# Performance work log

Measured on AMD Instinct MI355X. Metric: run time of the kernel, lower is better.

The kernel has to match this reference:

```python
import jax, jax.numpy as jnp
import numpy as np

B, T, D = 4, 2048, 512
H, DK = 4, 16
MU = 1.0


def _xavier(key, shape):
    lim = float(np.sqrt(6.0 / (shape[0] + shape[1])))
    return jax.random.uniform(key, shape, jnp.float32, -lim, lim)


def setup_inputs() -> dict:
    key = jax.random.key(0)
    ks = jax.random.split(key, 9)
    x = jax.random.normal(ks[0], (B, T, D), jnp.float32)
    Wq = _xavier(ks[1], (D, H * DK))
    Wk = _xavier(ks[2], (D, H * DK))
    Wv = _xavier(ks[3], (D, H * DK))
    # W_a is zero-initialized in the module; use small random values so the
    # decay path is exercised non-trivially.
    Wa = 0.02 * jax.random.normal(ks[4], (D, H), jnp.float32)
    ba = 0.02 * jax.random.normal(ks[5], (H,), jnp.float32)
    Wg = 0.02 * jax.random.normal(ks[6], (D, H * DK), jnp.float32)
    bg = jnp.zeros((H * DK,), jnp.float32)
    Wo = _xavier(ks[7], (H * DK, D))
    return {"x": x, "Wq": Wq, "Wk": Wk, "Wv": Wv, "Wa": Wa, "ba": ba,
            "Wg": Wg, "bg": bg, "Wo": Wo}


def reference(x, Wq, Wk, Wv, Wa, ba, Wg, bg, Wo):
    b_, t_, _ = x.shape
    q = (x @ Wq).reshape(b_, t_, H, DK)
    k = (x @ Wk).reshape(b_, t_, H, DK)
    v = (x @ Wv).reshape(b_, t_, H, DK)
    # bid b_s = <q_s, k_s>/sqrt(dk); decay a_s = -softplus(x W_a + c_a) <= 0
    bid = jnp.sum(q * k, axis=-1) / np.sqrt(DK)      # (B, T, H)
    a = -jax.nn.softplus(x @ Wa + ba)                # (B, T, H)
    # Closed form of the sequential scan:
    #   scores[t, s] = bid[s] + sum_{r=s+1..t} a[r] = (bid[s] - cumA[s]) + cumA[t]
    # Row-constant cumA[t] cancels in the softmax, so the attention weights are
    # a causal softmax over mu * (bid[s] - cumA[s]).
    cumA = jnp.cumsum(a, axis=1)                     # (B, T, H)
    lg = (bid - cumA).transpose(0, 2, 1)             # (B, H, S_keys)
    mask = jnp.tril(jnp.ones((t_, t_), bool))        # keys s <= query t
    scores = jnp.where(mask[None, None], MU * lg[:, :, None, :], -jnp.inf)
    w = jax.nn.softmax(scores, axis=-1)              # (B, H, T, S)
    y = jnp.einsum('bhts,bshd->bthd', w, v)          # (B, T, H, DK)
    gate = jax.nn.sigmoid(x @ Wg + bg).reshape(b_, t_, H, DK)
    y = (y * gate).reshape(b_, t_, H * DK)
    return y @ Wo
```

## Files before the change

kernel.cpp:

```cpp
#include <hip/hip_runtime.h>
#include <math.h>

#define B_    4
#define T_    2048
#define D_    512
#define H_    4
#define ROWS_ 8192
#define CHSZ_ 128
#define NCHK_ 16

typedef unsigned short ushort_t;
typedef unsigned int   uint_t;
typedef __attribute__((ext_vector_type(8))) __bf16         bfx8;
typedef __attribute__((ext_vector_type(8))) unsigned short u16x8;
typedef __attribute__((ext_vector_type(4))) float          fx4;

__device__ __forceinline__ ushort_t f2bf(float f) {
    union { float f; uint_t u; } v; v.f = f;
    return (ushort_t)((v.u + 0x7FFFu + ((v.u >> 16) & 1u)) >> 16);
}
__device__ __forceinline__ float bf2f(ushort_t u) {
    union { uint_t u; float f; } v; v.u = ((uint_t)u) << 16; return v.f;
}

__global__ __launch_bounds__(256) void prep_pack(const float* __restrict__ x,
                                                 const float* __restrict__ Wa,
                                                 const float* __restrict__ ba,
                                                 const float* __restrict__ Wq,
                                                 const float* __restrict__ Wk,
                                                 const float* __restrict__ Wv,
                                                 const float* __restrict__ Wg,
                                                 const float* __restrict__ Wo,
                                                 ushort_t* __restrict__ xbf,
                                                 float* __restrict__ Aarr,
                                                 ushort_t* __restrict__ WcatT2,
                                                 ushort_t* __restrict__ WoT) {
    const int blk = blockIdx.x;
    if (blk < 2048) {
        const int wave = threadIdx.x >> 6, lane = threadIdx.x & 63;
        const int row = blk * 4 + wave;
        const float* xp = x + (size_t)row * D_ + lane * 8;
        float4 f0 = *(const float4*)xp;
        float4 f1 = *(const float4*)(xp + 4);
        float xv[8] = {f0.x, f0.y, f0.z, f0.w, f1.x, f1.y, f1.z, f1.w};

        u16x8 u;
        #pragma unroll
        for (int j = 0; j < 8; j++) u[j] = f2bf(xv[j]);
        *(u16x8*)(xbf + (size_t)row * D_ + lane * 8) = u;

        float a0 = 0.f, a1 = 0.f, a2 = 0.f, a3 = 0.f;
        #pragma unroll
        for (int j = 0; j < 8; j++) {
            float4 w = *(const float4*)&Wa[(size_t)(lane * 8 + j) * 4];
            a0 = fmaf(xv[j], w.x, a0);
            a1 = fmaf(xv[j], w.y, a1);
            a2 = fmaf(xv[j], w.z, a2);
            a3 = fmaf(xv[j], w.w, a3);
        }
        #pragma unroll
        for (int off = 32; off; off >>= 1) {
            a0 += __shfl_xor(a0, off);
            a1 += __shfl_xor(a1, off);
            a2 += __shfl_xor(a2, off);
            a3 += __shfl_xor(a3, off);
        }
        if (lane == 0) {
            float z[4] = {a0 + ba[0], a1 + ba[1], a2 + ba[2], a3 + ba[3]};
            float r[4];
            #pragma unroll
            for (int h = 0; h < 4; h++)
                r[h] = -(fmaxf(z[h], 0.f) + log1pf(expf(-fabsf(z[h]))));
            *(float4*)&Aarr[(size_t)row * 4] = make_float4(r[0], r[1], r[2], r[3]);
        }
    } else {
        int idx = (blk - 2048) * 256 + threadIdx.x;
        if (idx < 256 * 512) {
            int n = idx >> 9, d = idx & 511;
            int h = n >> 6, r = n & 63, part = r >> 4, j = r & 15;
            int col = h * 16 + j;
            const float* W = (part == 0) ? Wq : (part == 1) ? Wk : (part == 2) ? Wv : Wg;
            WcatT2[idx] = f2bf(W[(size_t)d * 64 + col]);
        } else {
            int r = idx - 256 * 512;
            int n = r >> 6, k = r & 63;
            WoT[r] = f2bf(Wo[(size_t)k * 512 + n]);
        }
    }
}

__global__ __launch_bounds__(256) void gemm_scanA(const ushort_t* __restrict__ xbf,
                                                  const ushort_t* __restrict__ WcatT2,
                                                  const float* __restrict__ Aarr,
                                                  float* __restrict__ stateWS,
                                                  float* __restrict__ chunkSum,
                                                  ushort_t* __restrict__ gBuf) {
    __shared__ ushort_t As[128 * 72];
    __shared__ ushort_t Bs[64 * 72];
    __shared__ float s_a0;
    __shared__ float s_wmax[2];
    __shared__ float s_tot[17];

    const int rc = blockIdx.x & 63;
    const int h  = blockIdx.x >> 6;
    const int m0 = rc * 128;
    const int n0 = h * 64;
    const int b  = rc >> 4, chunk = rc & 15;
    const int bh = b * 4 + h;

    const int tid = threadIdx.x;
    const int wave = tid >> 6, lane = tid & 63;
    const int fr = lane & 15, quad = lane >> 4;
    const int sr = tid >> 3, sc = (tid & 7) * 8;

    fx4 acc[2][4];
    #pragma unroll
    for (int i = 0; i < 2; i++)
        #pragma unroll
        for (int j = 0; j < 4; j++) acc[i][j] = (fx4)0.f;

    u16x8 ra[4], rb[2];
    #pragma unroll
    for (int s = 0; s < 4; s++)
        ra[s] = *(const u16x8*)(xbf + (size_t)(m0 + s * 32 + sr) * D_ + sc);
    #pragma unroll
    for (int s = 0; s < 2; s++)
        rb[s] = *(const u16x8*)(WcatT2 + (size_t)(n0 + s * 32 + sr) * D_ + sc);

    for (int it = 0; it < 8; it++) {
        #pragma unroll
        for (int s = 0; s < 4; s++) *(u16x8*)&As[(s * 32 + sr) * 72 + sc] = ra[s];
        #pragma unroll
        for (int s = 0; s < 2; s++) *(u16x8*)&Bs[(s * 32 + sr) * 72 + sc] = rb[s];
        __syncthreads();
        if (it < 7) {
            const int k0 = (it + 1) * 64;
            #pragma unroll
            for (int s = 0; s < 4; s++)
                ra[s] = *(const u16x8*)(xbf + (size_t)(m0 + s * 32 + sr) * D_ + k0 + sc);
            #pragma unroll
            for (int s = 0; s < 2; s++)
                rb[s] = *(const u16x8*)(WcatT2 + (size_t)(n0 + s * 32 + sr) * D_ + k0 + sc);
        }
        #pragma unroll
        for (int ks = 0; ks < 64; ks += 32) {
            bfx8 af[2], bfr[4];
            #pragma unroll
            for (int mi = 0; mi < 2; mi++)
                af[mi] = *(const bfx8*)&As[(wave * 32 + mi * 16 + fr) * 72 + ks + quad * 8];
            #pragma unroll
            for (int ni = 0; ni < 4; ni++)
                bfr[ni] = *(const bfx8*)&Bs[(ni * 16 + fr) * 72 + ks + quad * 8];
            #pragma unroll
            for (int mi = 0; mi < 2; mi++)
                #pragma unroll
                for (int ni = 0; ni < 4; ni++)
                    acc[mi][ni] = __builtin_amdgcn_mfma_f32_16x16x32_bf16(af[mi], bfr[ni], acc[mi][ni], 0, 0, 0);
        }
        __syncthreads();
    }

    #pragma unroll
    for (int mi = 0; mi < 2; mi++)
        #pragma unroll
        for (int ni = 0; ni < 4; ni++)
            #pragma unroll
            for (int r = 0; r < 4; r++) {
                int rl = wave * 32 + mi * 16 + quad * 4 + r;
                int cl = ni * 16 + fr;
                As[rl * 72 + cl] = f2bf(acc[mi][ni][r]);
            }
    __syncthreads();

    const bool active = (tid < 128);
    float bid = 0.f, a = 0.f;
    float v[16];
    if (active) {
        const ushort_t* ct = &As[tid * 72];
        u16x8 q0 = *(const u16x8*)(ct +  0), q1 = *(const u16x8*)(ct +  8);
        u16x8 k0 = *(const u16x8*)(ct + 16), k1 = *(const u16x8*)(ct + 24);
        u16x8 v0 = *(const u16x8*)(ct + 32), v1 = *(const u16x8*)(ct + 40);
        #pragma unroll
        for (int j = 0; j < 8; j++) {
            bid = fmaf(bf2f(q0[j]), bf2f(k0[j]), bid);
            bid = fmaf(bf2f(q1[j]), bf2f(k1[j]), bid);
            v[j]     = bf2f(v0[j]);
            v[8 + j] = bf2f(v1[j]);
        }
        bid *= 0.25f;
        a = Aarr[(size_t)(m0 + tid) * 4 + h];
    }

    float ca = a;
    #pragma unroll
    for (int off = 1; off < 64; off <<= 1) {
        float up = __shfl_up(ca, off);
        if (lane >= off) ca += up;
    }
    if (tid == 63) s_a0 = ca;
    __syncthreads();
    if (active && wave == 1) ca += s_a0;

    float lg = bid - ca;

    float Mw = active ? lg : -1e30f;
    #pragma unroll
    for (int off = 32; off; off >>= 1) Mw = fmaxf(Mw, __shfl_xor(Mw, off));
    if (active && lane == 0) s_wmax[wave] = Mw;
    __syncthreads();
    const float M0 = s_wmax[0], M1 = s_wmax[1];
    const float Mc = fmaxf(M0, M1);

    float d = active ? __expf(lg - Mw) : 0.f;
    float n[16];
    #pragma unroll
    for (int j = 0; j < 16; j++) n[j] = d * v[j];
    #pragma unroll
    for (int off = 1; off < 64; off <<= 1) {
        float ud = __shfl_up(d, off);
        float un[16];
        #pragma unroll
        for (int j = 0; j < 16; j++) un[j] = __shfl_up(n[j], off);
        if (lane >= off) {
            d += ud;
            #pragma unroll
            for (int j = 0; j < 16; j++) n[j] += un[j];
        }
    }
    if (tid == 63) {
        s_tot[0] = d;
        #pragma unroll
        for (int j = 0; j < 16; j++) s_tot[1 + j] = n[j];
    }
    __syncthreads();
    if (active && wave == 1) {
        float al = __expf(M0 - Mc), be = __expf(M1 - Mc);
        d = s_tot[0] * al + d * be;
        #pragma unroll
        for (int j = 0; j < 16; j++) n[j] = s_tot[1 + j] * al + n[j] * be;
    }
    const float myM = (wave == 0) ? M0 : Mc;

    if (active) {
        const int t = chunk * CHSZ_ + tid;
        const size_t eidx = (size_t)bh * T_ + t;
        stateWS[eidx] = myM;
        stateWS[32768 + eidx] = d;
        #pragma unroll
        for (int j = 0; j < 16; j++) stateWS[(size_t)(2 + j) * 32768 + eidx] = n[j];

        const ushort_t* ct = &As[tid * 72];
        u16x8 g0 = *(const u16x8*)(ct + 48), g1 = *(const u16x8*)(ct + 56);
        *(u16x8*)(gBuf + eidx * 16)     = g0;
        *(u16x8*)(gBuf + eidx * 16 + 8) = g1;

        if (tid == 127) {
            float* cs = chunkSum + (size_t)(bh * NCHK_ + chunk) * 20;
            cs[0] = Mc; cs[1] = d;
            #pragma unroll
            for (int j = 0; j < 16; j++) cs[2 + j] = n[j];
            cs[18] = ca;
        }
    }
}

__global__ __launch_bounds__(128) void scanBC(const float* __restrict__ stateWS,
                                              const float* __restrict__ chunkSum,
                                              const ushort_t* __restrict__ gBuf,
                                              const float* __restrict__ bg,
                                              ushort_t* __restrict__ Ybf) {
    __shared__ float sp[20];
    const int blk = blockIdx.x;
    const int bh = blk >> 4, chunk = blk & 15;
    const int b = bh >> 2, h = bh & 3;
    const int tid = threadIdx.x;

    if (tid == 0) {
        float M = -INFINITY, D = 0.f, N[16];
        #pragma unroll
        for (int j = 0; j < 16; j++) N[j] = 0.f;
        float pA = 0.f;
        for (int c = 0; c < chunk; c++) {
            const float* cs = chunkSum + (size_t)(bh * NCHK_ + c) * 20;
            float m = cs[0] - pA, d = cs[1];
            float mn = fmaxf(M, m);
            float al = __expf(M - mn), be = __expf(m - mn);
            D = D * al + d * be;
            #pragma unroll
            for (int j = 0; j < 16; j++) N[j] = N[j] * al + cs[2 + j] * be;
            M = mn;
            pA += cs[18];
        }
        sp[0] = M; sp[1] = D;
        #pragma unroll
        for (int j = 0; j < 16; j++) sp[2 + j] = N[j];
        sp[18] = pA;
    }
    __syncthreads();

    const int t = chunk * CHSZ_ + tid;
    const size_t eidx = (size_t)bh * T_ + t;
    float M = sp[0], D = sp[1], pA = sp[18];
    float m = stateWS[eidx] - pA;
    float d = stateWS[32768 + eidx];
    float mn = fmaxf(M, m);
    float al = __expf(M - mn), be = __expf(m - mn);
    float invd = 1.f / (D * al + d * be);

    u16x8 g0 = *(const u16x8*)(gBuf + eidx * 16);
    u16x8 g1 = *(const u16x8*)(gBuf + eidx * 16 + 8);
    u16x8 o0, o1;
    #pragma unroll
    for (int j = 0; j < 16; j++) {
        float Nj = sp[2 + j] * al + stateWS[(size_t)(2 + j) * 32768 + eidx] * be;
        float gpre = ((j < 8) ? bf2f(g0[j]) : bf2f(g1[j - 8])) + bg[h * 16 + j];
        float gate = 1.f / (1.f + __expf(-gpre));
        ushort_t yb = f2bf(Nj * invd * gate);
        if (j < 8) o0[j] = yb; else o1[j - 8] = yb;
    }
    const size_t row = (size_t)b * T_ + t;
    *(u16x8*)(Ybf + row * 64 + h * 16)     = o0;
    *(u16x8*)(Ybf + row * 64 + h * 16 + 8) = o1;
}

__global__ __launch_bounds__(256) void gemm_bt(const ushort_t* __restrict__ A,
                                               const ushort_t* __restrict__ BT,
                                               float* __restrict__ C,
                                               int M, int N, int K) {
    __shared__ ushort_t As[64 * 72];
    __shared__ ushort_t Bs[128 * 72];
    const int tid = threadIdx.x;
    const int wave = tid >> 6, lane = tid & 63;
    const int m0 = blockIdx.y * 64, n0 = blockIdx.x * 128;
    const int wr = wave >> 1, wc = wave & 1;

    fx4 acc[2][4];
    #pragma unroll
    for (int i = 0; i < 2; i++)
        #pragma unroll
        for (int j = 0; j < 4; j++) acc[i][j] = (fx4)0.f;

    const int sr = tid >> 3, sc = (tid & 7) * 8;

    for (int k0 = 0; k0 < K; k0 += 64) {
        #pragma unroll
        for (int s = 0; s < 2; s++) {
            int r = s * 32 + sr;
            *(u16x8*)&As[r * 72 + sc] = *(const u16x8*)(A + (size_t)(m0 + r) * K + k0 + sc);
        }
        #pragma unroll
        for (int s = 0; s < 4; s++) {
            int r = s * 32 + sr;
            *(u16x8*)&Bs[r * 72 + sc] = *(const u16x8*)(BT + (size_t)(n0 + r) * K + k0 + sc);
        }
        __syncthreads();
        const int fr = lane & 15, quad = lane >> 4;
        #pragma unroll
        for (int ks = 0; ks < 64; ks += 32) {
            bfx8 af[2], bfr[4];
            #pragma unroll
            for (int mi = 0; mi < 2; mi++)
                af[mi] = *(const bfx8*)&As[(wr * 32 + mi * 16 + fr) * 72 + ks + quad * 8];
            #pragma unroll
            for (int ni = 0; ni < 4; ni++)
                bfr[ni] = *(const bfx8*)&Bs[(wc * 64 + ni * 16 + fr) * 72 + ks + quad * 8];
            #pragma unroll
            for (int mi = 0; mi < 2; mi++)
                #pragma unroll
                for (int ni = 0; ni < 4; ni++)
                    acc[mi][ni] = __builtin_amdgcn_mfma_f32_16x16x32_bf16(af[mi], bfr[ni], acc[mi][ni], 0, 0, 0);
        }
        __syncthreads();
    }

    const int fr = lane & 15, quad = lane >> 4;
    #pragma unroll
    for (int mi = 0; mi < 2; mi++)
        #pragma unroll
        for (int ni = 0; ni < 4; ni++)
            #pragma unroll
            for (int r = 0; r < 4; r++) {
                int rr = m0 + wr * 32 + mi * 16 + quad * 4 + r;
                int cc = n0 + wc * 64 + ni * 16 + fr;
                C[(size_t)rr * N + cc] = acc[mi][ni][r];
            }
}

extern "C" void kernel_launch(void* const* d_in, const int* in_sizes, int n_in,
                              void* d_out, int out_size, void* d_ws, size_t ws_size,
                              hipStream_t stream) {
    const float* x  = (const float*)d_in[0];
    const float* Wq = (const float*)d_in[1];
    const float* Wk = (const float*)d_in[2];
    const float* Wv = (const float*)d_in[3];
    const float* Wa = (const float*)d_in[4];
    const float* ba = (const float*)d_in[5];
    const float* Wg = (const float*)d_in[6];
    const float* bg = (const float*)d_in[7];
    const float* Wo = (const float*)d_in[8];
    float* out = (float*)d_out;

    char* w = (char*)d_ws;
    ushort_t* xbf      = (ushort_t*)w;  w += (size_t)ROWS_ * D_ * 2;
    ushort_t* WcatT2   = (ushort_t*)w;  w += 256 * 512 * 2;
    ushort_t* WoT      = (ushort_t*)w;  w += 512 * 64 * 2;
    float*    Aarr     = (float*)w;     w += (size_t)ROWS_ * 4 * 4;
    float*    stateWS  = (float*)w;     w += (size_t)18 * 32768 * 4;
    float*    chunkSum = (float*)w;     w += 256 * 20 * 4;
    ushort_t* gBuf     = (ushort_t*)w;  w += (size_t)32768 * 16 * 2;
    ushort_t* Ybf      = (ushort_t*)w;  w += (size_t)ROWS_ * 64 * 2;

    prep_pack<<<2688, 256, 0, stream>>>(x, Wa, ba, Wq, Wk, Wv, Wg, Wo,
                                        xbf, Aarr, WcatT2, WoT);
    gemm_scanA<<<256, 256, 0, stream>>>(xbf, WcatT2, Aarr, stateWS, chunkSum, gBuf);
    scanBC<<<256, 128, 0, stream>>>(stateWS, chunkSum, gBuf, bg, Ybf);
    gemm_bt<<<dim3(4, 128), 256, 0, stream>>>(Ybf, WoT, out, ROWS_, D_, 64);
}
```

Measured before the change: 118.0 us.

## Fuse cross-chunk scan combine into output projection GEMM

```diff
diff --git a/kernel.cpp b/kernel.cpp
--- a/kernel.cpp
+++ b/kernel.cpp
@@ -264,125 +264,138 @@
     }
 }
 
-__global__ __launch_bounds__(128) void scanBC(const float* __restrict__ stateWS,
-                                              const float* __restrict__ chunkSum,
-                                              const ushort_t* __restrict__ gBuf,
-                                              const float* __restrict__ bg,
-                                              ushort_t* __restrict__ Ybf) {
-    __shared__ float sp[20];
-    const int blk = blockIdx.x;
-    const int bh = blk >> 4, chunk = blk & 15;
-    const int b = bh >> 2, h = bh & 3;
+__global__ __launch_bounds__(256) void scan_gemm(const float* __restrict__ stateWS,
+                                                 const float* __restrict__ chunkSum,
+                                                 const ushort_t* __restrict__ gBuf,
+                                                 const float* __restrict__ bg,
+                                                 const ushort_t* __restrict__ WoT,
+                                                 float* __restrict__ C) {
+    __shared__ ushort_t Ys[64 * 72];
+    __shared__ ushort_t Bs[128 * 72];
+    __shared__ float s_pref[4][18];
+
+    const int m0 = blockIdx.y * 64;
+    const int n0 = blockIdx.x * 128;
+    const int b  = m0 >> 11;
+    const int tt = m0 & 2047;
+    const int chunk = tt >> 7;
+
     const int tid = threadIdx.x;
-
-    if (tid == 0) {
-        float M = -INFINITY, D = 0.f, N[16];
-        #pragma unroll
-        for (int j = 0; j < 16; j++) N[j] = 0.f;
-        float pA = 0.f;
-        for (int c = 0; c < chunk; c++) {
-            const float* cs = chunkSum + (size_t)(bh * NCHK_ + c) * 20;
-            float m = cs[0] - pA, d = cs[1];
-            float mn = fmaxf(M, m);
-            float al = __expf(M - mn), be = __expf(m - mn);
-            D = D * al + d * be;
-            #pragma unroll
-            for (int j = 0; j < 16; j++) N[j] = N[j] * al + cs[2 + j] * be;
-            M = mn;
-            pA += cs[18];
-        }
-        sp[0] = M; sp[1] = D;
-        #pragma unroll
-        for (int j = 0; j < 16; j++) sp[2 + j] = N[j];
-        sp[18] = pA;
-    }
-    __syncthreads();
-
-    const int t = chunk * CHSZ_ + tid;
-    const size_t eidx = (size_t)bh * T_ + t;
-    float M = sp[0], D = sp[1], pA = sp[18];
-    float m = stateWS[eidx] - pA;
-    float d = stateWS[32768 + eidx];
-    float mn = fmaxf(M, m);
-    float al = __expf(M - mn), be = __expf(m - mn);
-    float invd = 1.f / (D * al + d * be);
-
+    const int wave = tid >> 6, lane = tid & 63;
+
+    const int sr = tid >> 3, sc = (tid & 7) * 8;
+    #pragma unroll
+    for (int s = 0; s < 4; s++) {
+        int rr = s * 32 + sr;
+        *(u16x8*)&Bs[rr * 72 + sc] = *(const u16x8*)(WoT + (size_t)(n0 + rr) * 64 + sc);
+    }
+
+    const int h = wave, r = lane;
+    const int bh = b * 4 + h;
+    const size_t eidx = (size_t)bh * T_ + tt + r;
+    float m_row = stateWS[eidx];
+    float d_row = stateWS[32768 + eidx];
+    float n_row[16];
+    #pragma unroll
+    for (int j = 0; j < 16; j++) n_row[j] = stateWS[(size_t)(2 + j) * 32768 + eidx];
     u16x8 g0 = *(const u16x8*)(gBuf + eidx * 16);
     u16x8 g1 = *(const u16x8*)(gBuf + eidx * 16 + 8);
-    u16x8 o0, o1;
-    #pragma unroll
-    for (int j = 0; j < 16; j++) {
-        float Nj = sp[2 + j] * al + stateWS[(size_t)(2 + j) * 32768 + eidx] * be;
-        float gpre = ((j < 8) ? bf2f(g0[j]) : bf2f(g1[j - 8])) + bg[h * 16 + j];
-        float gate = 1.f / (1.f + __expf(-gpre));
-        ushort_t yb = f2bf(Nj * invd * gate);
-        if (j < 8) o0[j] = yb; else o1[j - 8] = yb;
-    }
-    const size_t row = (size_t)b * T_ + t;
-    *(u16x8*)(Ybf + row * 64 + h * 16)     = o0;
-    *(u16x8*)(Ybf + row * 64 + h * 16 + 8) = o1;
-}
-
-__global__ __launch_bounds__(256) void gemm_bt(const ushort_t* __restrict__ A,
-                                               const ushort_t* __restrict__ BT,
-                                               float* __restrict__ C,
-                                               int M, int N, int K) {
-    __shared__ ushort_t As[64 * 72];
-    __shared__ ushort_t Bs[128 * 72];
-    const int tid = threadIdx.x;
-    const int wave = tid >> 6, lane = tid & 63;
-    const int m0 = blockIdx.y * 64, n0 = blockIdx.x * 128;
+
+    if (wave == 0) {
+        const int hh = lane >> 4, p = lane & 15;
+        const int bhh = b * 4 + hh;
+        float mf = -1e30f, dd = 0.f, aT = 0.f;
+        float nn[16];
+        #pragma unroll
+        for (int j = 0; j < 16; j++) nn[j] = 0.f;
+        if (p < chunk) {
+            const float* cs = chunkSum + (size_t)(bhh * NCHK_ + p) * 20;
+            mf = cs[0]; dd = cs[1];
+            #pragma unroll
+            for (int j = 0; j < 16; j++) nn[j] = cs[2 + j];
+            aT = cs[18];
+        }
+        float off = aT;
+        #pragma unroll
+        for (int s = 1; s < 16; s <<= 1) {
+            float t2 = __shfl_down(off, s, 16);
+            if (p + s < chunk) off += t2;
+        }
+        if (p < chunk) mf += off;
+        #pragma unroll
+        for (int s = 1; s < 16; s <<= 1) {
+            float m2 = __shfl_xor(mf, s, 16);
+            float d2 = __shfl_xor(dd, s, 16);
+            float mx = fmaxf(mf, m2);
+            float al = __expf(mf - mx), be = __expf(m2 - mx);
+            #pragma unroll
+            for (int j = 0; j < 16; j++) {
+                float n2 = __shfl_xor(nn[j], s, 16);
+                nn[j] = nn[j] * al + n2 * be;
+            }
+            dd = dd * al + d2 * be;
+            mf = mx;
+        }
+        if (p == 0) {
+            s_pref[hh][0] = mf; s_pref[hh][1] = dd;
+            #pragma unroll
+            for (int j = 0; j < 16; j++) s_pref[hh][2 + j] = nn[j];
+        }
+    }
+    __syncthreads();
+
+    {
+        const float M = s_pref[h][0], D = s_pref[h][1];
+        const float mx = fmaxf(M, m_row);
+        const float al = __expf(M - mx), be = __expf(m_row - mx);
+        const float invd = 1.f / (D * al + d_row * be);
+        u16x8 o0, o1;
+        #pragma unroll
+        for (int j = 0; j < 16; j++) {
+            float Nj = s_pref[h][2 + j] * al + n_row[j] * be;
+            float gpre = ((j < 8) ? bf2f(g0[j]) : bf2f(g1[j - 8])) + bg[h * 16 + j];
+            float gate = 1.f / (1.f + __expf(-gpre));
+            ushort_t yb = f2bf(Nj * invd * gate);
+            if (j < 8) o0[j] = yb; else o1[j - 8] = yb;
+        }
+        *(u16x8*)&Ys[r * 72 + h * 16]     = o0;
+        *(u16x8*)&Ys[r * 72 + h * 16 + 8] = o1;
+    }
+    __syncthreads();
+
     const int wr = wave >> 1, wc = wave & 1;
-
+    const int fr = lane & 15, quad = lane >> 4;
     fx4 acc[2][4];
     #pragma unroll
     for (int i = 0; i < 2; i++)
         #pragma unroll
         for (int j = 0; j < 4; j++) acc[i][j] = (fx4)0.f;
 
-    const int sr = tid >> 3, sc = (tid & 7) * 8;
-
-    for (int k0 = 0; k0 < K; k0 += 64) {
-        #pragma unroll
-        for (int s = 0; s < 2; s++) {
-            int r = s * 32 + sr;
-            *(u16x8*)&As[r * 72 + sc] = *(const u16x8*)(A + (size_t)(m0 + r) * K + k0 + sc);
-        }
-        #pragma unroll
-        for (int s = 0; s < 4; s++) {
-            int r = s * 32 + sr;
-            *(u16x8*)&Bs[r * 72 + sc] = *(const u16x8*)(BT + (size_t)(n0 + r) * K + k0 + sc);
-        }
-        __syncthreads();
-        const int fr = lane & 15, quad = lane >> 4;
-        #pragma unroll
-        for (int ks = 0; ks < 64; ks += 32) {
-            bfx8 af[2], bfr[4];
-            #pragma unroll
-            for (int mi = 0; mi < 2; mi++)
-                af[mi] = *(const bfx8*)&As[(wr * 32 + mi * 16 + fr) * 72 + ks + quad * 8];
+    #pragma unroll
+    for (int ks = 0; ks < 64; ks += 32) {
+        bfx8 af[2], bfr[4];
+        #pragma unroll
+        for (int mi = 0; mi < 2; mi++)
+            af[mi] = *(const bfx8*)&Ys[(wr * 32 + mi * 16 + fr) * 72 + ks + quad * 8];
+        #pragma unroll
+        for (int ni = 0; ni < 4; ni++)
+            bfr[ni] = *(const bfx8*)&Bs[(wc * 64 + ni * 16 + fr) * 72 + ks + quad * 8];
+        #pragma unroll
+        for (int mi = 0; mi < 2; mi++)
             #pragma unroll
             for (int ni = 0; ni < 4; ni++)
-                bfr[ni] = *(const bfx8*)&Bs[(wc * 64 + ni * 16 + fr) * 72 + ks + quad * 8];
-            #pragma unroll
-            for (int mi = 0; mi < 2; mi++)
-                #pragma unroll
-                for (int ni = 0; ni < 4; ni++)
-                    acc[mi][ni] = __builtin_amdgcn_mfma_f32_16x16x32_bf16(af[mi], bfr[ni], acc[mi][ni], 0, 0, 0);
-        }
-        __syncthreads();
-    }
-
-    const int fr = lane & 15, quad = lane >> 4;
+                acc[mi][ni] = __builtin_amdgcn_mfma_f32_16x16x32_bf16(af[mi], bfr[ni], acc[mi][ni], 0, 0, 0);
+    }
+
     #pragma unroll
     for (int mi = 0; mi < 2; mi++)
         #pragma unroll
         for (int ni = 0; ni < 4; ni++)
             #pragma unroll
-            for (int r = 0; r < 4; r++) {
-                int rr = m0 + wr * 32 + mi * 16 + quad * 4 + r;
-                int cc = n0 + wc * 64 + ni * 16 + fr;
-                C[(size_t)rr * N + cc] = acc[mi][ni][r];
+            for (int rr = 0; rr < 4; rr++) {
+                int orow = m0 + wr * 32 + mi * 16 + quad * 4 + rr;
+                int ocol = n0 + wc * 64 + ni * 16 + fr;
+                C[(size_t)orow * D_ + ocol] = acc[mi][ni][rr];
             }
 }
 
@@ -408,11 +421,9 @@
     float*    stateWS  = (float*)w;     w += (size_t)18 * 32768 * 4;
     float*    chunkSum = (float*)w;     w += 256 * 20 * 4;
     ushort_t* gBuf     = (ushort_t*)w;  w += (size_t)32768 * 16 * 2;
-    ushort_t* Ybf      = (ushort_t*)w;  w += (size_t)ROWS_ * 64 * 2;
 
     prep_pack<<<2688, 256, 0, stream>>>(x, Wa, ba, Wq, Wk, Wv, Wg, Wo,
                                         xbf, Aarr, WcatT2, WoT);
     gemm_scanA<<<256, 256, 0, stream>>>(xbf, WcatT2, Aarr, stateWS, chunkSum, gBuf);
-    scanBC<<<256, 128, 0, stream>>>(stateWS, chunkSum, gBuf, bg, Ybf);
-    gemm_bt<<<dim3(4, 128), 256, 0, stream>>>(Ybf, WoT, out, ROWS_, D_, 64);
-}
+    scan_gemm<<<dim3(4, 128), 256, 0, stream>>>(stateWS, chunkSum, gBuf, bg, WoT, out);
+}
```

Result: faster. 111.5 us (-5.5%).
